# Kernel tuning notes

Hardware: AMD Instinct MI355X
Metric: run time of the kernel (lower is better)

Reference implementation:

```python
import jax, jax.numpy as jnp
import numpy as np

H = 128   # hidden_size
C = 80    # number of classes / per-class GRUs


def setup_inputs():
    key = jax.random.key(0)
    ks = jax.random.split(key, 16)
    lengths = np.array([100 + 4 * j for j in range(C)], dtype=np.int64)   # ragged segment sizes
    ucl = np.concatenate([np.zeros(1, np.int64), np.cumsum(lengths)])     # [C+1] boundaries
    N = int(ucl[-1])                                                      # 20640 total boxes
    r = jax.random.normal
    return {
        "boxes_feature": r(ks[0], (N, 1024), jnp.float32),
        "boxes_score": r(ks[1], (N, 32), jnp.float32),
        "boxes_box": r(ks[2], (N, 4), jnp.float32),
        "all_class_boxes_feature": r(ks[3], (N, 1024), jnp.float32),
        "all_class_boxes_score": r(ks[4], (N, 32), jnp.float32),
        "all_class_boxes_box": r(ks[5], (N, 32), jnp.float32),
        "all_class_boxes_origin_score": r(ks[6], (N, 32), jnp.float32),
        "unique_class": np.ones(C, dtype=np.int64),
        "unique_class_len": ucl,
        "appear_W": r(ks[7], (H, 1024), jnp.float32) / np.sqrt(1024.0).astype(np.float32),
        "appear_b": jnp.zeros((H,), jnp.float32),
        "feat_W": r(ks[8], (H, H + 96), jnp.float32) / np.sqrt(float(H + 96)).astype(np.float32),
        "feat_b": jnp.zeros((H,), jnp.float32),
        "gru_Wih": r(ks[9], (C, 2, 3 * H, H), jnp.float32) / np.sqrt(float(H)).astype(np.float32),
        "gru_Whh": r(ks[10], (C, 2, 3 * H, H), jnp.float32) / np.sqrt(float(H)).astype(np.float32),
        "gru_bih": r(ks[11], (C, 2, 3 * H), jnp.float32) * 0.01,
        "gru_bhh": r(ks[12], (C, 2, 3 * H), jnp.float32) * 0.01,
        "out_W": r(ks[13], (1, 2 * H), jnp.float32) / np.sqrt(2.0 * H).astype(np.float32),
        "out_b": jnp.zeros((1,), jnp.float32),
    }


def _forward(all_class_boxes_feature, all_class_boxes_score, all_class_boxes_box,
             all_class_boxes_origin_score, unique_class, unique_class_len,
             appear_W, appear_b, feat_W, feat_b,
             gru_Wih, gru_Whh, gru_bih, gru_bhh, out_W, out_b):
    # --- static ragged bookkeeping (int inputs are concrete numpy) ---
    ucl = np.asarray(unique_class_len)
    lengths = ucl[1:] - ucl[:-1]                                   # [C]
    starts = ucl[:-1]
    L = int(lengths.max())
    t = np.arange(L)
    mask = jnp.asarray(t[None, :] < lengths[:, None])              # [C,L] valid-position mask
    gidx = jnp.asarray(starts[:, None] + np.minimum(t[None, :], lengths[:, None] - 1))  # [C,L]
    ridx = jnp.asarray(np.clip(lengths[:, None] - 1 - t[None, :], 0, None))             # [C,L]

    # --- shared feature pipeline ---
    feat = jax.nn.relu(all_class_boxes_feature @ appear_W.T + appear_b)   # [N,H]
    allf = jnp.concatenate([feat, all_class_boxes_score, all_class_boxes_box,
                            all_class_boxes_origin_score], axis=1)        # [N,H+96]
    dec = jax.nn.relu(allf @ feat_W.T + feat_b)                           # [N,H]

    X = dec[gidx]                                                  # [C,L,H] padded per-class segments
    Xr = jnp.take_along_axis(X, ridx[:, :, None], axis=1)          # time-reversed within each length

    def run_dir(Xd, Wih, Whh, bih, bhh):
        # precompute input projections; scan only carries the hidden recurrence
        Xp = jnp.einsum('clh,cgh->clg', Xd, Wih) + bih[:, None, :]  # [C,L,3H]

        def per_class(xp, m, Whh_c, bhh_c):
            def step(h, inp):
                x_t, m_t = inp
                gh = Whh_c @ h + bhh_c
                r = jax.nn.sigmoid(x_t[:H] + gh[:H])                # PyTorch gate order r,z,n
                z = jax.nn.sigmoid(x_t[H:2 * H] + gh[H:2 * H])
                n = jnp.tanh(x_t[2 * H:] + r * gh[2 * H:])
                h2 = jnp.where(m_t, (1.0 - z) * n + z * h, h)
                return h2, h2
            _, out = jax.lax.scan(step, jnp.zeros((H,), xp.dtype), (xp, m))
            return out                                              # [L,H]
        return jax.vmap(per_class)(Xp, mask, Whh, bhh)              # [C,L,H]

    out_f = run_dir(X, gru_Wih[:, 0], gru_Whh[:, 0], gru_bih[:, 0], gru_bhh[:, 0])
    out_r = run_dir(Xr, gru_Wih[:, 1], gru_Whh[:, 1], gru_bih[:, 1], gru_bhh[:, 1])
    out_bd = jnp.take_along_axis(out_r, ridx[:, :, None], axis=1)   # un-reverse backward outputs
    Y = jnp.concatenate([out_f, out_bd], axis=-1)                   # [C,L,2H]

    # flatten valid positions back to the original box order (segments are contiguous)
    seg = jnp.asarray(np.repeat(np.arange(C), lengths))
    loc = jnp.asarray(np.concatenate([np.arange(int(l)) for l in lengths]))
    flat = Y[seg, loc]                                              # [N,2H]
    return jax.nn.sigmoid(flat @ out_W.T + out_b)[:, None, :]       # [N,1,1] like torch output


def reference(boxes_feature, boxes_score, boxes_box, all_class_boxes_feature,
              all_class_boxes_score, all_class_boxes_box, all_class_boxes_origin_score,
              unique_class, unique_class_len, appear_W, appear_b, feat_W, feat_b,
              gru_Wih, gru_Whh, gru_bih, gru_bhh, out_W, out_b):
    # boxes_feature/boxes_score/boxes_box are accepted but unused, as in the torch forward
    return _forward(all_class_boxes_feature, all_class_boxes_score, all_class_boxes_box,
                    all_class_boxes_origin_score, unique_class, unique_class_len,
                    appear_W, appear_b, feat_W, feat_b,
                    gru_Wih, gru_Whh, gru_bih, gru_bhh, out_W, out_b)
```

## Files before the change

kernel.cpp:

```cpp
#include <hip/hip_runtime.h>
#include <hip/hip_bf16.h>
#include <cstdint>


typedef _Float16 half2_t __attribute__((ext_vector_type(2)));
typedef _Float16 half8_t __attribute__((ext_vector_type(8)));

__device__ __forceinline__ void lds_barrier() {
    asm volatile("s_waitcnt lgkmcnt(0)\n\ts_barrier" ::: "memory");
}

__global__ __launch_bounds__(256) void concat_kernel(
    const float* __restrict__ score, const float* __restrict__ box,
    const float* __restrict__ orig, float* __restrict__ allf, int N)
{
    int idx = blockIdx.x * 256 + threadIdx.x;
    int total = N * 96;
    if (idx >= total) return;
    int n = idx / 96, j = idx - n * 96;
    float v;
    if (j < 32)      v = score[(size_t)n * 32 + j];
    else if (j < 64) v = box  [(size_t)n * 32 + j - 32];
    else             v = orig [(size_t)n * 32 + j - 64];
    allf[(size_t)n * 224 + 128 + j] = v;
}

__global__ __launch_bounds__(256) void gemm128_kernel(
    const float* __restrict__ A, int lda,
    const float* __restrict__ B,
    const float* __restrict__ bias,
    float* __restrict__ Cc, int ldc,
    int N, int K, int do_relu)
{
    __shared__ __align__(16) float As[16][64];
    __shared__ __align__(16) float Bs[16][128];
    const int tid = threadIdx.x;
    const int tx = tid & 15, ty = tid >> 4;
    const int n0 = blockIdx.x * 64;
    const int arow = tid >> 2;

    float acc[4][8] = {};

    int ar = n0 + arow; if (ar > N - 1) ar = N - 1;
    const float* Aptr  = A + (size_t)ar * lda + (tid & 3) * 4;
    const int m0 = tid >> 2;
    const int kq4 = (tid & 3) * 4;
    const float* Bptr0 = B + (size_t)m0 * K + (tid & 3) * 4;
    const float* Bptr1 = Bptr0 + (size_t)64 * K;

    float4 av = *(const float4*)(Aptr);
    float4 b0 = *(const float4*)(Bptr0);
    float4 b1 = *(const float4*)(Bptr1);

    for (int kb = 0; kb < K; kb += 16) {
        lds_barrier();
        As[kq4 + 0][arow] = av.x;
        As[kq4 + 1][arow] = av.y;
        As[kq4 + 2][arow] = av.z;
        As[kq4 + 3][arow] = av.w;
        Bs[kq4 + 0][m0] = b0.x; Bs[kq4 + 1][m0] = b0.y;
        Bs[kq4 + 2][m0] = b0.z; Bs[kq4 + 3][m0] = b0.w;
        Bs[kq4 + 0][m0 + 64] = b1.x; Bs[kq4 + 1][m0 + 64] = b1.y;
        Bs[kq4 + 2][m0 + 64] = b1.z; Bs[kq4 + 3][m0 + 64] = b1.w;
        lds_barrier();
        if (kb + 16 < K) {
            av = *(const float4*)(Aptr + kb + 16);
            b0 = *(const float4*)(Bptr0 + kb + 16);
            b1 = *(const float4*)(Bptr1 + kb + 16);
        }
        #pragma unroll
        for (int kk = 0; kk < 16; kk++) {
            float4 a = *(const float4*)&As[kk][ty * 4];
            float4 p = *(const float4*)&Bs[kk][tx * 8];
            float4 q = *(const float4*)&Bs[kk][tx * 8 + 4];
            float av4[4] = {a.x, a.y, a.z, a.w};
            float bv[8]  = {p.x, p.y, p.z, p.w, q.x, q.y, q.z, q.w};
            #pragma unroll
            for (int i = 0; i < 4; i++)
                #pragma unroll
                for (int j = 0; j < 8; j++)
                    acc[i][j] = fmaf(av4[i], bv[j], acc[i][j]);
        }
    }

    #pragma unroll
    for (int i = 0; i < 4; i++) {
        int row = n0 + ty * 4 + i;
        if (row >= N) continue;
        float o[8];
        #pragma unroll
        for (int j = 0; j < 8; j++) {
            float v = acc[i][j] + bias[tx * 8 + j];
            if (do_relu) v = v > 0.f ? v : 0.f;
            o[j] = v;
        }
        float4* dst = (float4*)(Cc + (size_t)row * ldc + tx * 8);
        dst[0] = make_float4(o[0], o[1], o[2], o[3]);
        dst[1] = make_float4(o[4], o[5], o[6], o[7]);
    }
}

__global__ __launch_bounds__(256) void xp_kernel(
    const float* __restrict__ dec,
    const float* __restrict__ Wih,
    const float* __restrict__ bih,
    const int* __restrict__ ucl,
    float* __restrict__ xp,
    int N)
{
    const int c = blockIdx.x;
    const int tile = blockIdx.y;
    const int d  = blockIdx.z / 3;
    const int mt = blockIdx.z % 3;
    const int start = ucl[c];
    const int len = ucl[c + 1] - start;
    const int t0 = tile * 64;
    if (t0 >= len) return;

    __shared__ __align__(16) float As[16][64];
    __shared__ __align__(16) float Bs[16][128];
    const int tid = threadIdx.x;
    const int tx = tid & 15, ty = tid >> 4;
    const int arow = tid >> 2;

    int t = t0 + arow; if (t > len - 1) t = len - 1;
    int srow = start + (d ? (len - 1 - t) : t);
    const float* Aptr = dec + (size_t)srow * 128 + (tid & 3) * 4;

    const float* Bbase = Wih + ((size_t)(c * 2 + d) * 384 + mt * 128) * 128;
    const int m0 = tid >> 2;
    const int kq4 = (tid & 3) * 4;
    const float* Bptr0 = Bbase + (size_t)m0 * 128 + (tid & 3) * 4;
    const float* Bptr1 = Bptr0 + (size_t)64 * 128;

    float4 av = *(const float4*)(Aptr);
    float4 b0 = *(const float4*)(Bptr0);
    float4 b1 = *(const float4*)(Bptr1);

    float acc[4][8] = {};
    for (int kb = 0; kb < 128; kb += 16) {
        lds_barrier();
        As[kq4 + 0][arow] = av.x;
        As[kq4 + 1][arow] = av.y;
        As[kq4 + 2][arow] = av.z;
        As[kq4 + 3][arow] = av.w;
        Bs[kq4 + 0][m0] = b0.x; Bs[kq4 + 1][m0] = b0.y;
        Bs[kq4 + 2][m0] = b0.z; Bs[kq4 + 3][m0] = b0.w;
        Bs[kq4 + 0][m0 + 64] = b1.x; Bs[kq4 + 1][m0 + 64] = b1.y;
        Bs[kq4 + 2][m0 + 64] = b1.z; Bs[kq4 + 3][m0 + 64] = b1.w;
        lds_barrier();
        if (kb + 16 < 128) {
            av = *(const float4*)(Aptr + kb + 16);
            b0 = *(const float4*)(Bptr0 + kb + 16);
            b1 = *(const float4*)(Bptr1 + kb + 16);
        }
        #pragma unroll
        for (int kk = 0; kk < 16; kk++) {
            float4 a = *(const float4*)&As[kk][ty * 4];
            float4 p = *(const float4*)&Bs[kk][tx * 8];
            float4 q = *(const float4*)&Bs[kk][tx * 8 + 4];
            float av4[4] = {a.x, a.y, a.z, a.w};
            float bv[8]  = {p.x, p.y, p.z, p.w, q.x, q.y, q.z, q.w};
            #pragma unroll
            for (int i = 0; i < 4; i++)
                #pragma unroll
                for (int j = 0; j < 8; j++)
                    acc[i][j] = fmaf(av4[i], bv[j], acc[i][j]);
        }
    }

    const float* bias = bih + (size_t)(c * 2 + d) * 384 + mt * 128;
    #pragma unroll
    for (int i = 0; i < 4; i++) {
        int tt = t0 + ty * 4 + i;
        if (tt >= len) continue;
        float o[8];
        #pragma unroll
        for (int j = 0; j < 8; j++) o[j] = acc[i][j] + bias[tx * 8 + j];
        float4* dst = (float4*)(xp + ((size_t)d * N + start + tt) * 384 + mt * 128 + tx * 8);
        dst[0] = make_float4(o[0], o[1], o[2], o[3]);
        dst[1] = make_float4(o[4], o[5], o[6], o[7]);
    }
}

__global__ __launch_bounds__(128, 1) void gru_kernel(
    const float* __restrict__ xp,
    const float* __restrict__ Whh,
    const float* __restrict__ bhh,
    const int* __restrict__ ucl,
    float* __restrict__ outY,
    int N)
{
    const int c = blockIdx.x, d = blockIdx.y;
    const int start = ucl[c];
    const int len = ucl[c + 1] - start;
    const int g = threadIdx.x;

    const float* wbase = Whh + (size_t)(c * 2 + d) * 384 * 128;
    half2_t w0[64], w1[64], w2[64];
    {
        const float2* r0 = (const float2*)(wbase + (size_t)g * 128);
        const float2* r1 = (const float2*)(wbase + (size_t)(g + 128) * 128);
        const float2* r2 = (const float2*)(wbase + (size_t)(g + 256) * 128);
        #pragma unroll
        for (int i = 0; i < 64; i++) {
            float2 a = r0[i];
            w0[i] = half2_t{(_Float16)a.x, (_Float16)a.y};
        }
        #pragma unroll
        for (int i = 0; i < 64; i++) {
            float2 a = r1[i];
            w1[i] = half2_t{(_Float16)a.x, (_Float16)a.y};
        }
        #pragma unroll
        for (int i = 0; i < 64; i++) {
            float2 a = r2[i];
            w2[i] = half2_t{(_Float16)a.x, (_Float16)a.y};
        }
    }
    const float* bb = bhh + (size_t)(c * 2 + d) * 384;
    const float bh0 = bb[g], bh1 = bb[g + 128], bh2 = bb[g + 256];

    __shared__ __align__(16) half2_t hbuf[2][64];
    if (g < 64) { hbuf[0][g] = half2_t{(_Float16)0.f, (_Float16)0.f}; }
    const float* xpb = xp + ((size_t)d * N + start) * 384;
    float* outb = outY + (size_t)start * 256 + d * 128;

    float xa0 = xpb[g], xa1 = xpb[g + 128], xa2 = xpb[g + 256];
    const size_t o1 = (size_t)((len > 1) ? 1 : 0) * 384;
    float xb0 = xpb[o1 + g], xb1 = xpb[o1 + g + 128], xb2 = xpb[o1 + g + 256];
    float hcur = 0.f;
    lds_barrier();

#define GRU_SUBSTEP(HP_IDX, HN_IDX, X0, X1, X2, TT)                          \
    {                                                                        \
        const half8_t* __restrict__ hp = (const half8_t*)hbuf[HP_IDX];       \
        _Float16* __restrict__ hn = (_Float16*)hbuf[HN_IDX];                 \
        float a0 = bh0, a1 = bh1, a2 = bh2;                                  \
        half8_t hr[4];                                                       \
        hr[0] = hp[0]; hr[1] = hp[1]; hr[2] = hp[2]; hr[3] = hp[3];          \
        _Pragma("unroll")                                                    \
        for (int i = 0; i < 16; i++) {                                       \
            union { half8_t v; half2_t h2[4]; } u;                           \
            u.v = hr[i & 3];                                                 \
            if (i + 4 < 16) hr[i & 3] = hp[i + 4];   \
            _Pragma("unroll")                                                \
            for (int j = 0; j < 4; j++) {                                    \
                a0 = __builtin_amdgcn_fdot2(w0[i * 4 + j], u.h2[j], a0, false);\
                a1 = __builtin_amdgcn_fdot2(w1[i * 4 + j], u.h2[j], a1, false);\
                a2 = __builtin_amdgcn_fdot2(w2[i * 4 + j], u.h2[j], a2, false);\
            }                                                                \
        }                                                                    \
        float r = __fdividef(1.f, 1.f + __expf(-((X0) + a0)));               \
        float z = __fdividef(1.f, 1.f + __expf(-((X1) + a1)));               \
        float pre = (X2) + r * a2;                                           \
        float n = 1.f - __fdividef(2.f, __expf(2.f * pre) + 1.f);            \
        float hnew = (1.f - z) * n + z * hcur;                               \
        hn[g] = (_Float16)hnew;                                              \
        hcur = hnew;                                                         \
        outb[(size_t)(TT) * 256 + g] = hnew;                                 \
    }

    for (int t = 0; t < len; t += 2) {
        int tpa = (t + 2 < len) ? (t + 2) : (len - 1);
        const float* xra = xpb + (size_t)tpa * 384;
        float ta0 = xra[g], ta1 = xra[g + 128], ta2 = xra[g + 256];
        int ttA = d ? (len - 1 - t) : t;
        GRU_SUBSTEP(0, 1, xa0, xa1, xa2, ttA)
        xa0 = ta0; xa1 = ta1; xa2 = ta2;
        lds_barrier();
        if (t + 1 >= len) break;
        int tpb = (t + 3 < len) ? (t + 3) : (len - 1);
        const float* xrb = xpb + (size_t)tpb * 384;
        float tb0 = xrb[g], tb1 = xrb[g + 128], tb2 = xrb[g + 256];
        int ttB = d ? (len - 2 - t) : (t + 1);
        GRU_SUBSTEP(1, 0, xb0, xb1, xb2, ttB)
        xb0 = tb0; xb1 = tb1; xb2 = tb2;
        lds_barrier();
    }
#undef GRU_SUBSTEP
}

__global__ __launch_bounds__(256) void final_kernel(
    const float* __restrict__ outY,
    const float* __restrict__ outW,
    const float* __restrict__ outb,
    float* __restrict__ out, int N)
{
    __shared__ __align__(16) float wsh[256];
    wsh[threadIdx.x] = outW[threadIdx.x];
    __syncthreads();
    const int lane = threadIdx.x & 63;
    const int wave = (blockIdx.x * 256 + threadIdx.x) >> 6;
    const int nw = gridDim.x * 4;
    float4 w4 = *(const float4*)&wsh[lane * 4];
    float b = outb[0];
    for (int n = wave; n < N; n += nw) {
        float4 y = *(const float4*)(outY + (size_t)n * 256 + lane * 4);
        float p = y.x * w4.x + y.y * w4.y + y.z * w4.z + y.w * w4.w;
        #pragma unroll
        for (int off = 32; off > 0; off >>= 1) p += __shfl_down(p, off);
        if (lane == 0) out[n] = 1.f / (1.f + __expf(-(p + b)));
    }
}

extern "C" void kernel_launch(void* const* d_in, const int* in_sizes, int n_in,
                              void* d_out, int out_size, void* d_ws, size_t ws_size,
                              hipStream_t stream)
{
    const float* acbf  = (const float*)d_in[3];
    const float* score = (const float*)d_in[4];
    const float* box   = (const float*)d_in[5];
    const float* orig  = (const float*)d_in[6];
    const int*   ucl   = (const int*)d_in[8];
    const float* aW  = (const float*)d_in[9];
    const float* ab  = (const float*)d_in[10];
    const float* fW  = (const float*)d_in[11];
    const float* fb  = (const float*)d_in[12];
    const float* Wih = (const float*)d_in[13];
    const float* Whh = (const float*)d_in[14];
    const float* bih = (const float*)d_in[15];
    const float* bhh = (const float*)d_in[16];
    const float* oW  = (const float*)d_in[17];
    const float* ob  = (const float*)d_in[18];
    float* out = (float*)d_out;

    const int N = in_sizes[3] / 1024;
    const int C = in_sizes[7];

    float* ws   = (float*)d_ws;
    float* allf = ws;
    float* dec  = ws + (size_t)N * 224;
    float* xp   = dec + (size_t)N * 128;
    float* outY = ws;

    dim3 blk(256);
    concat_kernel<<<dim3((N * 96 + 255) / 256), blk, 0, stream>>>(score, box, orig, allf, N);
    gemm128_kernel<<<dim3((N + 63) / 64), blk, 0, stream>>>(acbf, 1024, aW, ab, allf, 224, N, 1024, 1);
    gemm128_kernel<<<dim3((N + 63) / 64), blk, 0, stream>>>(allf, 224, fW, fb, dec, 128, N, 224, 1);
    xp_kernel<<<dim3(C, 7, 6), blk, 0, stream>>>(dec, Wih, bih, ucl, xp, N);
    gru_kernel<<<dim3(C, 2), dim3(128), 0, stream>>>(xp, Whh, bhh, ucl, outY, N);
    final_kernel<<<dim3(160), blk, 0, stream>>>(outY, oW, ob, out, N);
}
```

Baseline: 695.3 us.

## Use fp16 MFMA for projection GEMMs and store intermediates in fp16

Replaces the scalar-FMA fp32 tiled GEMMs (appearance, feature, and per-class input projections) with kernels built on mfma_f32_16x16x32_f16, converting fp32 inputs and weights to half on load. Intermediate buffers (concatenated features, decoder activations, GRU input projections) are now stored as fp16, halving their memory traffic, and the GRU reads fp16 input projections. The aim is to cut GEMM compute time and bandwidth in the stages ahead of the sequential GRU. This adds precision loss from fp16 intermediates, and the output stores are scattered 2-byte writes that are not vectorized.

```diff
diff --git a/kernel.cpp b/kernel.cpp
--- a/kernel.cpp
+++ b/kernel.cpp
@@ -5,14 +5,20 @@
 
 typedef _Float16 half2_t __attribute__((ext_vector_type(2)));
 typedef _Float16 half8_t __attribute__((ext_vector_type(8)));
+typedef float f32x4 __attribute__((ext_vector_type(4)));
 
 __device__ __forceinline__ void lds_barrier() {
     asm volatile("s_waitcnt lgkmcnt(0)\n\ts_barrier" ::: "memory");
 }
 
+__device__ __forceinline__ half8_t cvt8(float4 f0, float4 f1) {
+    return half8_t{(_Float16)f0.x, (_Float16)f0.y, (_Float16)f0.z, (_Float16)f0.w,
+                   (_Float16)f1.x, (_Float16)f1.y, (_Float16)f1.z, (_Float16)f1.w};
+}
+
 __global__ __launch_bounds__(256) void concat_kernel(
     const float* __restrict__ score, const float* __restrict__ box,
-    const float* __restrict__ orig, float* __restrict__ allf, int N)
+    const float* __restrict__ orig, _Float16* __restrict__ allf, int N)
 {
     int idx = blockIdx.x * 256 + threadIdx.x;
     int total = N * 96;
@@ -22,169 +28,159 @@
     if (j < 32)      v = score[(size_t)n * 32 + j];
     else if (j < 64) v = box  [(size_t)n * 32 + j - 32];
     else             v = orig [(size_t)n * 32 + j - 64];
-    allf[(size_t)n * 224 + 128 + j] = v;
-}
-
-__global__ __launch_bounds__(256) void gemm128_kernel(
-    const float* __restrict__ A, int lda,
-    const float* __restrict__ B,
+    allf[(size_t)n * 224 + 128 + j] = (_Float16)v;
+}
+
+template<bool A_F16>
+__global__ __launch_bounds__(256) void mfma_gemm_kernel(
+    const void* __restrict__ Av, int lda,
+    const float* __restrict__ B, int ldb,
     const float* __restrict__ bias,
-    float* __restrict__ Cc, int ldc,
-    int N, int K, int do_relu)
-{
-    __shared__ __align__(16) float As[16][64];
-    __shared__ __align__(16) float Bs[16][128];
+    _Float16* __restrict__ Cc, int ldc,
+    int Nrows, int K, int do_relu)
+{
+    __shared__ __align__(16) _Float16 Asl[256 * 8];
+    __shared__ __align__(16) _Float16 Bsl[512 * 8];
     const int tid = threadIdx.x;
-    const int tx = tid & 15, ty = tid >> 4;
+    const int wave = tid >> 6, lane = tid & 63;
     const int n0 = blockIdx.x * 64;
-    const int arow = tid >> 2;
-
-    float acc[4][8] = {};
-
-    int ar = n0 + arow; if (ar > N - 1) ar = N - 1;
-    const float* Aptr  = A + (size_t)ar * lda + (tid & 3) * 4;
-    const int m0 = tid >> 2;
-    const int kq4 = (tid & 3) * 4;
-    const float* Bptr0 = B + (size_t)m0 * K + (tid & 3) * 4;
-    const float* Bptr1 = Bptr0 + (size_t)64 * K;
-
-    float4 av = *(const float4*)(Aptr);
-    float4 b0 = *(const float4*)(Bptr0);
-    float4 b1 = *(const float4*)(Bptr1);
-
-    for (int kb = 0; kb < K; kb += 16) {
-        lds_barrier();
-        As[kq4 + 0][arow] = av.x;
-        As[kq4 + 1][arow] = av.y;
-        As[kq4 + 2][arow] = av.z;
-        As[kq4 + 3][arow] = av.w;
-        Bs[kq4 + 0][m0] = b0.x; Bs[kq4 + 1][m0] = b0.y;
-        Bs[kq4 + 2][m0] = b0.z; Bs[kq4 + 3][m0] = b0.w;
-        Bs[kq4 + 0][m0 + 64] = b1.x; Bs[kq4 + 1][m0 + 64] = b1.y;
-        Bs[kq4 + 2][m0 + 64] = b1.z; Bs[kq4 + 3][m0 + 64] = b1.w;
-        lds_barrier();
-        if (kb + 16 < K) {
-            av = *(const float4*)(Aptr + kb + 16);
-            b0 = *(const float4*)(Bptr0 + kb + 16);
-            b1 = *(const float4*)(Bptr1 + kb + 16);
-        }
-        #pragma unroll
-        for (int kk = 0; kk < 16; kk++) {
-            float4 a = *(const float4*)&As[kk][ty * 4];
-            float4 p = *(const float4*)&Bs[kk][tx * 8];
-            float4 q = *(const float4*)&Bs[kk][tx * 8 + 4];
-            float av4[4] = {a.x, a.y, a.z, a.w};
-            float bv[8]  = {p.x, p.y, p.z, p.w, q.x, q.y, q.z, q.w};
-            #pragma unroll
-            for (int i = 0; i < 4; i++)
-                #pragma unroll
-                for (int j = 0; j < 8; j++)
-                    acc[i][j] = fmaf(av4[i], bv[j], acc[i][j]);
-        }
-    }
-
+
+    const int a_rt = tid >> 6, a_q = (tid >> 4) & 3, a_m = tid & 15;
+    int arow = n0 + a_rt * 16 + a_m; if (arow > Nrows - 1) arow = Nrows - 1;
+    const int b_q = (tid >> 4) & 3, b_n = tid & 15;
+    const int bcol0 = (tid >> 6) * 16 + b_n;
+    const int bcol1 = bcol0 + 64;
+
+    f32x4 acc[8] = {};
+    half8_t a_st, b_st0, b_st1;
+
+    auto load_chunk = [&](int kc) {
+        int k = kc * 32;
+        if constexpr (A_F16) {
+            const _Float16* A = (const _Float16*)Av;
+            a_st = *(const half8_t*)(A + (size_t)arow * lda + k + a_q * 8);
+        } else {
+            const float* A = (const float*)Av;
+            const float4* p = (const float4*)(A + (size_t)arow * lda + k + a_q * 8);
+            a_st = cvt8(p[0], p[1]);
+        }
+        const float4* p0 = (const float4*)(B + (size_t)bcol0 * ldb + k + b_q * 8);
+        const float4* p1 = (const float4*)(B + (size_t)bcol1 * ldb + k + b_q * 8);
+        b_st0 = cvt8(p0[0], p0[1]);
+        b_st1 = cvt8(p1[0], p1[1]);
+    };
+
+    load_chunk(0);
+    const int nkc = K >> 5;
+    for (int kc = 0; kc < nkc; kc++) {
+        lds_barrier();
+        *(half8_t*)(Asl + tid * 8) = a_st;
+        *(half8_t*)(Bsl + tid * 8) = b_st0;
+        *(half8_t*)(Bsl + (tid + 256) * 8) = b_st1;
+        lds_barrier();
+        if (kc + 1 < nkc) load_chunk(kc + 1);
+        half8_t af = *(const half8_t*)(Asl + (wave * 64 + lane) * 8);
+        #pragma unroll
+        for (int ct = 0; ct < 8; ct++) {
+            half8_t bf = *(const half8_t*)(Bsl + (ct * 64 + lane) * 8);
+            acc[ct] = __builtin_amdgcn_mfma_f32_16x16x32_f16(af, bf, acc[ct], 0, 0, 0);
+        }
+    }
+
+    const int crow = n0 + wave * 16 + (lane >> 4) * 4;
+    const int ccol = lane & 15;
     #pragma unroll
-    for (int i = 0; i < 4; i++) {
-        int row = n0 + ty * 4 + i;
-        if (row >= N) continue;
-        float o[8];
-        #pragma unroll
-        for (int j = 0; j < 8; j++) {
-            float v = acc[i][j] + bias[tx * 8 + j];
+    for (int ct = 0; ct < 8; ct++) {
+        int col = ct * 16 + ccol;
+        float bv = bias[col];
+        #pragma unroll
+        for (int reg = 0; reg < 4; reg++) {
+            int row = crow + reg;
+            if (row >= Nrows) continue;
+            float v = acc[ct][reg] + bv;
             if (do_relu) v = v > 0.f ? v : 0.f;
-            o[j] = v;
-        }
-        float4* dst = (float4*)(Cc + (size_t)row * ldc + tx * 8);
-        dst[0] = make_float4(o[0], o[1], o[2], o[3]);
-        dst[1] = make_float4(o[4], o[5], o[6], o[7]);
-    }
-}
-
-__global__ __launch_bounds__(256) void xp_kernel(
-    const float* __restrict__ dec,
+            Cc[(size_t)row * ldc + col] = (_Float16)v;
+        }
+    }
+}
+
+__global__ __launch_bounds__(256) void mfma_xp_kernel(
+    const _Float16* __restrict__ dec,
     const float* __restrict__ Wih,
     const float* __restrict__ bih,
     const int* __restrict__ ucl,
-    float* __restrict__ xp,
+    _Float16* __restrict__ xp,
     int N)
 {
     const int c = blockIdx.x;
     const int tile = blockIdx.y;
-    const int d  = blockIdx.z / 3;
-    const int mt = blockIdx.z % 3;
+    const int d = blockIdx.z / 3, mt = blockIdx.z % 3;
     const int start = ucl[c];
     const int len = ucl[c + 1] - start;
     const int t0 = tile * 64;
     if (t0 >= len) return;
 
-    __shared__ __align__(16) float As[16][64];
-    __shared__ __align__(16) float Bs[16][128];
+    __shared__ __align__(16) _Float16 Asl[256 * 8];
+    __shared__ __align__(16) _Float16 Bsl[512 * 8];
     const int tid = threadIdx.x;
-    const int tx = tid & 15, ty = tid >> 4;
-    const int arow = tid >> 2;
-
-    int t = t0 + arow; if (t > len - 1) t = len - 1;
-    int srow = start + (d ? (len - 1 - t) : t);
-    const float* Aptr = dec + (size_t)srow * 128 + (tid & 3) * 4;
-
-    const float* Bbase = Wih + ((size_t)(c * 2 + d) * 384 + mt * 128) * 128;
-    const int m0 = tid >> 2;
-    const int kq4 = (tid & 3) * 4;
-    const float* Bptr0 = Bbase + (size_t)m0 * 128 + (tid & 3) * 4;
-    const float* Bptr1 = Bptr0 + (size_t)64 * 128;
-
-    float4 av = *(const float4*)(Aptr);
-    float4 b0 = *(const float4*)(Bptr0);
-    float4 b1 = *(const float4*)(Bptr1);
-
-    float acc[4][8] = {};
-    for (int kb = 0; kb < 128; kb += 16) {
-        lds_barrier();
-        As[kq4 + 0][arow] = av.x;
-        As[kq4 + 1][arow] = av.y;
-        As[kq4 + 2][arow] = av.z;
-        As[kq4 + 3][arow] = av.w;
-        Bs[kq4 + 0][m0] = b0.x; Bs[kq4 + 1][m0] = b0.y;
-        Bs[kq4 + 2][m0] = b0.z; Bs[kq4 + 3][m0] = b0.w;
-        Bs[kq4 + 0][m0 + 64] = b1.x; Bs[kq4 + 1][m0 + 64] = b1.y;
-        Bs[kq4 + 2][m0 + 64] = b1.z; Bs[kq4 + 3][m0 + 64] = b1.w;
-        lds_barrier();
-        if (kb + 16 < 128) {
-            av = *(const float4*)(Aptr + kb + 16);
-            b0 = *(const float4*)(Bptr0 + kb + 16);
-            b1 = *(const float4*)(Bptr1 + kb + 16);
-        }
-        #pragma unroll
-        for (int kk = 0; kk < 16; kk++) {
-            float4 a = *(const float4*)&As[kk][ty * 4];
-            float4 p = *(const float4*)&Bs[kk][tx * 8];
-            float4 q = *(const float4*)&Bs[kk][tx * 8 + 4];
-            float av4[4] = {a.x, a.y, a.z, a.w};
-            float bv[8]  = {p.x, p.y, p.z, p.w, q.x, q.y, q.z, q.w};
-            #pragma unroll
-            for (int i = 0; i < 4; i++)
-                #pragma unroll
-                for (int j = 0; j < 8; j++)
-                    acc[i][j] = fmaf(av4[i], bv[j], acc[i][j]);
+    const int wave = tid >> 6, lane = tid & 63;
+
+    const int a_rt = tid >> 6, a_q = (tid >> 4) & 3, a_m = tid & 15;
+    int t = t0 + a_rt * 16 + a_m; if (t > len - 1) t = len - 1;
+    const int srow = start + (d ? (len - 1 - t) : t);
+
+    const float* Bb = Wih + ((size_t)(c * 2 + d) * 384 + mt * 128) * 128;
+    const int b_q = (tid >> 4) & 3, b_n = tid & 15;
+    const int bcol0 = (tid >> 6) * 16 + b_n;
+    const int bcol1 = bcol0 + 64;
+
+    f32x4 acc[8] = {};
+    half8_t a_st, b_st0, b_st1;
+
+    auto load_chunk = [&](int kc) {
+        int k = kc * 32;
+        a_st = *(const half8_t*)(dec + (size_t)srow * 128 + k + a_q * 8);
+        const float4* p0 = (const float4*)(Bb + (size_t)bcol0 * 128 + k + b_q * 8);
+        const float4* p1 = (const float4*)(Bb + (size_t)bcol1 * 128 + k + b_q * 8);
+        b_st0 = cvt8(p0[0], p0[1]);
+        b_st1 = cvt8(p1[0], p1[1]);
+    };
+
+    load_chunk(0);
+    for (int kc = 0; kc < 4; kc++) {
+        lds_barrier();
+        *(half8_t*)(Asl + tid * 8) = a_st;
+        *(half8_t*)(Bsl + tid * 8) = b_st0;
+        *(half8_t*)(Bsl + (tid + 256) * 8) = b_st1;
+        lds_barrier();
+        if (kc + 1 < 4) load_chunk(kc + 1);
+        half8_t af = *(const half8_t*)(Asl + (wave * 64 + lane) * 8);
+        #pragma unroll
+        for (int ct = 0; ct < 8; ct++) {
+            half8_t bf = *(const half8_t*)(Bsl + (ct * 64 + lane) * 8);
+            acc[ct] = __builtin_amdgcn_mfma_f32_16x16x32_f16(af, bf, acc[ct], 0, 0, 0);
         }
     }
 
     const float* bias = bih + (size_t)(c * 2 + d) * 384 + mt * 128;
+    const int trow = t0 + wave * 16 + (lane >> 4) * 4;
+    const int ccol = lane & 15;
     #pragma unroll
-    for (int i = 0; i < 4; i++) {
-        int tt = t0 + ty * 4 + i;
-        if (tt >= len) continue;
-        float o[8];
-        #pragma unroll
-        for (int j = 0; j < 8; j++) o[j] = acc[i][j] + bias[tx * 8 + j];
-        float4* dst = (float4*)(xp + ((size_t)d * N + start + tt) * 384 + mt * 128 + tx * 8);
-        dst[0] = make_float4(o[0], o[1], o[2], o[3]);
-        dst[1] = make_float4(o[4], o[5], o[6], o[7]);
+    for (int ct = 0; ct < 8; ct++) {
+        int col = ct * 16 + ccol;
+        float bv = bias[col];
+        #pragma unroll
+        for (int reg = 0; reg < 4; reg++) {
+            int tt = trow + reg;
+            if (tt >= len) continue;
+            float v = acc[ct][reg] + bv;
+            xp[((size_t)d * N + start + tt) * 384 + mt * 128 + col] = (_Float16)v;
+        }
     }
 }
 
 __global__ __launch_bounds__(128, 1) void gru_kernel(
-    const float* __restrict__ xp,
+    const _Float16* __restrict__ xp,
     const float* __restrict__ Whh,
     const float* __restrict__ bhh,
     const int* __restrict__ ucl,
@@ -223,12 +219,12 @@
 
     __shared__ __align__(16) half2_t hbuf[2][64];
     if (g < 64) { hbuf[0][g] = half2_t{(_Float16)0.f, (_Float16)0.f}; }
-    const float* xpb = xp + ((size_t)d * N + start) * 384;
+    const _Float16* xpb = xp + ((size_t)d * N + start) * 384;
     float* outb = outY + (size_t)start * 256 + d * 128;
 
-    float xa0 = xpb[g], xa1 = xpb[g + 128], xa2 = xpb[g + 256];
+    float xa0 = (float)xpb[g], xa1 = (float)xpb[g + 128], xa2 = (float)xpb[g + 256];
     const size_t o1 = (size_t)((len > 1) ? 1 : 0) * 384;
-    float xb0 = xpb[o1 + g], xb1 = xpb[o1 + g + 128], xb2 = xpb[o1 + g + 256];
+    float xb0 = (float)xpb[o1 + g], xb1 = (float)xpb[o1 + g + 128], xb2 = (float)xpb[o1 + g + 256];
     float hcur = 0.f;
     lds_barrier();
 
@@ -243,7 +239,7 @@
         for (int i = 0; i < 16; i++) {                                       \
             union { half8_t v; half2_t h2[4]; } u;                           \
             u.v = hr[i & 3];                                                 \
-            if (i + 4 < 16) hr[i & 3] = hp[i + 4];   \
+            if (i + 4 < 16) hr[i & 3] = hp[i + 4];                           \
             _Pragma("unroll")                                                \
             for (int j = 0; j < 4; j++) {                                    \
                 a0 = __builtin_amdgcn_fdot2(w0[i * 4 + j], u.h2[j], a0, false);\
@@ -263,16 +259,16 @@
 
     for (int t = 0; t < len; t += 2) {
         int tpa = (t + 2 < len) ? (t + 2) : (len - 1);
-        const float* xra = xpb + (size_t)tpa * 384;
-        float ta0 = xra[g], ta1 = xra[g + 128], ta2 = xra[g + 256];
+        const _Float16* xra = xpb + (size_t)tpa * 384;
+        float ta0 = (float)xra[g], ta1 = (float)xra[g + 128], ta2 = (float)xra[g + 256];
         int ttA = d ? (len - 1 - t) : t;
         GRU_SUBSTEP(0, 1, xa0, xa1, xa2, ttA)
         xa0 = ta0; xa1 = ta1; xa2 = ta2;
         lds_barrier();
         if (t + 1 >= len) break;
         int tpb = (t + 3 < len) ? (t + 3) : (len - 1);
-        const float* xrb = xpb + (size_t)tpb * 384;
-        float tb0 = xrb[g], tb1 = xrb[g + 128], tb2 = xrb[g + 256];
+        const _Float16* xrb = xpb + (size_t)tpb * 384;
+        float tb0 = (float)xrb[g], tb1 = (float)xrb[g + 128], tb2 = (float)xrb[g + 256];
         int ttB = d ? (len - 2 - t) : (t + 1);
         GRU_SUBSTEP(1, 0, xb0, xb1, xb2, ttB)
         xb0 = tb0; xb1 = tb1; xb2 = tb2;
@@ -328,17 +324,19 @@
     const int N = in_sizes[3] / 1024;
     const int C = in_sizes[7];
 
-    float* ws   = (float*)d_ws;
-    float* allf = ws;
-    float* dec  = ws + (size_t)N * 224;
-    float* xp   = dec + (size_t)N * 128;
-    float* outY = ws;
+    _Float16* allf16 = (_Float16*)d_ws;
+    _Float16* dec16  = allf16 + (size_t)N * 224;
+    _Float16* xp16   = dec16 + (size_t)N * 128;
+    float*    outY   = (float*)(xp16 + (size_t)2 * N * 384);
 
     dim3 blk(256);
-    concat_kernel<<<dim3((N * 96 + 255) / 256), blk, 0, stream>>>(score, box, orig, allf, N);
-    gemm128_kernel<<<dim3((N + 63) / 64), blk, 0, stream>>>(acbf, 1024, aW, ab, allf, 224, N, 1024, 1);
-    gemm128_kernel<<<dim3((N + 63) / 64), blk, 0, stream>>>(allf, 224, fW, fb, dec, 128, N, 224, 1);
-    xp_kernel<<<dim3(C, 7, 6), blk, 0, stream>>>(dec, Wih, bih, ucl, xp, N);
-    gru_kernel<<<dim3(C, 2), dim3(128), 0, stream>>>(xp, Whh, bhh, ucl, outY, N);
+    const int rowblocks = (N + 63) / 64;
+    concat_kernel<<<dim3((N * 96 + 255) / 256), blk, 0, stream>>>(score, box, orig, allf16, N);
+    mfma_gemm_kernel<false><<<dim3(rowblocks), blk, 0, stream>>>(
+        (const void*)acbf, 1024, aW, 1024, ab, allf16, 224, N, 1024, 1);
+    mfma_gemm_kernel<true><<<dim3(rowblocks), blk, 0, stream>>>(
+        (const void*)allf16, 224, fW, 224, fb, dec16, 128, N, 224, 1);
+    mfma_xp_kernel<<<dim3(C, 7, 6), blk, 0, stream>>>(dec16, Wih, bih, ucl, xp16, N);
+    gru_kernel<<<dim3(C, 2), dim3(128), 0, stream>>>(xp16, Whh, bhh, ucl, outY, N);
     final_kernel<<<dim3(160), blk, 0, stream>>>(outY, oW, ob, out, N);
 }
```

After: 607.8 us. -12.6%, faster.
